# Optimization experiments

Measured on AMD Instinct MI355X. Metric: run time of the kernel, lower is better.

Reference implementation:

```python
import jax, jax.numpy as jnp
import numpy as np
from math import sqrt

B, S, D, H = 2, 2048, 1024, 16
HD = D // H


def setup_inputs() -> dict:
    key = jax.random.key(0)
    ks = jax.random.split(key, 5)
    std = 0.02
    return {
        "tensor_in": jax.random.normal(ks[0], (B, S, D), dtype=jnp.float32),
        "attention_mask": jnp.zeros((1, 1, S, S), dtype=jnp.float32),
        "Wq": jax.random.normal(ks[1], (D, D), dtype=jnp.float32) * std,
        "Wk": jax.random.normal(ks[2], (D, D), dtype=jnp.float32) * std,
        "Wv": jax.random.normal(ks[3], (D, D), dtype=jnp.float32) * std,
        "Wo": jax.random.normal(ks[4], (D, D), dtype=jnp.float32) * std,
    }


def reference(tensor_in, attention_mask, Wq, Wk, Wv, Wo):
    # nn.Linear(dim, dim, bias=False): y = x @ W.T, W is [out, in]
    q = tensor_in @ Wq.T  # [B,S,D]
    k = tensor_in @ Wk.T
    v = tensor_in @ Wv.T
    # split heads -> [B,H,S,HD]
    q = q.reshape(B, S, H, HD).transpose(0, 2, 1, 3)
    k = k.reshape(B, S, H, HD).transpose(0, 2, 1, 3)
    v = v.reshape(B, S, H, HD).transpose(0, 2, 1, 3)
    # scores [B,H,S,S]; note: mask added BEFORE scaling, scale = sqrt(full dim)
    scores = jnp.einsum("bhqd,bhkd->bhqk", q, k) + attention_mask
    weights = jax.nn.softmax(scores / sqrt(D), axis=-1)  # dropout = identity (eval)
    context = jnp.einsum("bhqk,bhkd->bhqd", weights, v)
    context = context.transpose(0, 2, 1, 3).reshape(B, S, D)
    return context @ Wo.T
```

## Files before the change

### kernel.cpp

```cpp
#include <hip/hip_runtime.h>

#define B_  2
#define S_  2048
#define D_  1024
#define H_  16
#define HD_ 64
#define M_  (B_*S_)

typedef __attribute__((ext_vector_type(8))) short  short8;
typedef __attribute__((ext_vector_type(4))) float  float4v;
typedef __attribute__((ext_vector_type(4))) int    int4v;
typedef __attribute__((ext_vector_type(4))) unsigned short ushort4v;

#define QSCALE 0.03125f

__device__ __forceinline__ unsigned short f_to_bf16bits(float f) {
    unsigned int x = __builtin_bit_cast(unsigned int, f);
    unsigned int lsb = (x >> 16) & 1u;
    x += 0x7fffu + lsb;
    return (unsigned short)(x >> 16);
}

__device__ __forceinline__ void async16(unsigned short* lds, const unsigned short* g) {
    __builtin_amdgcn_global_load_lds(
        (const __attribute__((address_space(1))) void*)g,
        (__attribute__((address_space(3))) void*)lds, 16, 0, 0);
}

__global__ __launch_bounds__(256) void cvt_bf16(
    const float* __restrict__ X,  const float* __restrict__ Wq,
    const float* __restrict__ Wk, const float* __restrict__ Wv,
    const float* __restrict__ Wo,
    unsigned short* __restrict__ Xb,  unsigned short* __restrict__ Wqb,
    unsigned short* __restrict__ Wkb, unsigned short* __restrict__ Wvb,
    unsigned short* __restrict__ Wob)
{
    const long t = (long)blockIdx.x * 256 + threadIdx.x;
    const long e = t * 8;
    const float* src; unsigned short* dst; long off;
    if      (e < 4194304) { src = X;  dst = Xb;  off = e; }
    else if (e < 5242880) { src = Wq; dst = Wqb; off = e - 4194304; }
    else if (e < 6291456) { src = Wk; dst = Wkb; off = e - 5242880; }
    else if (e < 7340032) { src = Wv; dst = Wvb; off = e - 6291456; }
    else                  { src = Wo; dst = Wob; off = e - 7340032; }
    float4v a = *(const float4v*)&src[off];
    float4v b = *(const float4v*)&src[off + 4];
    int4v o;
    o[0] = (int)f_to_bf16bits(a[0]) | ((int)f_to_bf16bits(a[1]) << 16);
    o[1] = (int)f_to_bf16bits(a[2]) | ((int)f_to_bf16bits(a[3]) << 16);
    o[2] = (int)f_to_bf16bits(b[0]) | ((int)f_to_bf16bits(b[1]) << 16);
    o[3] = (int)f_to_bf16bits(b[2]) | ((int)f_to_bf16bits(b[3]) << 16);
    *(int4v*)&dst[off] = o;
}

__global__ __launch_bounds__(256) void gemm_bt(
    const unsigned short* __restrict__ A,
    const unsigned short* __restrict__ B0,
    const unsigned short* __restrict__ B1,
    const unsigned short* __restrict__ B2,
    void* __restrict__ O0, void* __restrict__ O1, void* __restrict__ O2,
    int mode_base)
{
    const int K = 1024;
    const int z = blockIdx.z;
    const unsigned short* Bw = (z == 0) ? B0 : (z == 1) ? B1 : B2;
    void* Op                 = (z == 0) ? O0 : (z == 1) ? O1 : O2;
    const int mode = mode_base + z;

    __shared__ alignas(16) unsigned short As[128 * 32];
    __shared__ alignas(16) unsigned short Bs[128 * 32];

    const int tid  = threadIdx.x;
    const int wv   = tid >> 6;
    const int lane = tid & 63;
    const int wm   = wv >> 1, wn = wv & 1;
    const int q4   = lane >> 4, l15 = lane & 15;

    const int m0 = blockIdx.x * 128;
    const int n0 = blockIdx.y * 128;

    const int r0 = (wv * 2 + 0) * 16 + (lane >> 2);
    const int r1 = (wv * 2 + 1) * 16 + (lane >> 2);
    const int c0 = (((lane & 3) ^ (r0 & 3)) * 8);
    const int c1 = (((lane & 3) ^ (r1 & 3)) * 8);
    const unsigned short* gA0 = A  + (long)(m0 + r0) * K + c0;
    const unsigned short* gA1 = A  + (long)(m0 + r1) * K + c1;
    const unsigned short* gB0 = Bw + (long)(n0 + r0) * K + c0;
    const unsigned short* gB1 = Bw + (long)(n0 + r1) * K + c1;
    const int slot0 = (wv * 2 + 0) * 512;
    const int slot1 = (wv * 2 + 1) * 512;

    const int swz = (q4 ^ (l15 & 3)) * 8;
    int aoff[4], boff[4];
#pragma unroll
    for (int t = 0; t < 4; t++) {
        aoff[t] = (wm * 64 + t * 16 + l15) * 32 + swz;
        boff[t] = (wn * 64 + t * 16 + l15) * 32 + swz;
    }

    float4v acc[4][4];
#pragma unroll
    for (int i = 0; i < 4; i++)
#pragma unroll
        for (int j = 0; j < 4; j++) acc[i][j] = (float4v)0.0f;

    for (int k0 = 0; k0 < K; k0 += 32) {
        __syncthreads();
        async16(&As[slot0], gA0); async16(&As[slot1], gA1);
        async16(&Bs[slot0], gB0); async16(&Bs[slot1], gB1);
        gA0 += 32; gA1 += 32; gB0 += 32; gB1 += 32;
        __syncthreads();

        short8 afr[4], bfr[4];
#pragma unroll
        for (int mt = 0; mt < 4; mt++) afr[mt] = *(const short8*)&As[aoff[mt]];
#pragma unroll
        for (int nt = 0; nt < 4; nt++) bfr[nt] = *(const short8*)&Bs[boff[nt]];
#pragma unroll
        for (int mt = 0; mt < 4; mt++)
#pragma unroll
            for (int nt = 0; nt < 4; nt++)
                acc[mt][nt] = __builtin_amdgcn_mfma_f32_16x16x32_bf16(
                    afr[mt], bfr[nt], acc[mt][nt], 0, 0, 0);
    }

#pragma unroll
    for (int mt = 0; mt < 4; mt++)
#pragma unroll
        for (int nt = 0; nt < 4; nt++)
#pragma unroll
            for (int r = 0; r < 4; r++) {
                const int m = m0 + wm * 64 + mt * 16 + q4 * 4 + r;
                const int n = n0 + wn * 64 + nt * 16 + l15;
                float v = acc[mt][nt][r];
                if (mode == 3) {
                    ((float*)Op)[(long)m * D_ + n] = v;
                } else {
                    long off;
                    if (mode != 2)
                        off = ((long)((m >> 11) * H_ + (n >> 6)) * S_ + (m & 2047)) * HD_ + (n & 63);
                    else
                        off = ((long)((m >> 11) * H_ + (n >> 6)) * HD_ + (n & 63)) * S_ + (m & 2047);
                    if (mode == 0) v *= QSCALE;
                    ((unsigned short*)Op)[off] = f_to_bf16bits(v);
                }
            }
}

__global__ __launch_bounds__(256) void attn(
    const unsigned short* __restrict__ Q,
    const unsigned short* __restrict__ Kk,
    const unsigned short* __restrict__ Vt,
    const float* __restrict__ mask,
    unsigned short* __restrict__ ctx)
{
    __shared__ alignas(16) unsigned short Ks [64 * 72];
    __shared__ alignas(16) unsigned short Vts[64 * 72];
    __shared__ alignas(16) unsigned short Ps [4][16 * 72];

    const int tid  = threadIdx.x;
    const int wv   = tid >> 6;
    const int lane = tid & 63;
    const int q4   = lane >> 4, l15 = lane & 15;
    const int bh   = blockIdx.y;
    const int q0   = blockIdx.x * 64;

    const long head = (long)bh * S_ * HD_;

    const int qrow = q0 + wv * 16 + l15;
    short8 qfr[2];
    qfr[0] = *(const short8*)&Q[head + (long)qrow * HD_ + q4 * 8];
    qfr[1] = *(const short8*)&Q[head + (long)qrow * HD_ + 32 + q4 * 8];

    float l_acc[4];
#pragma unroll
    for (int r = 0; r < 4; r++) l_acc[r] = 0.0f;
    float4v oacc[4];
#pragma unroll
    for (int dt = 0; dt < 4; dt++) oacc[dt] = (float4v)0.0f;

    const int lrow = tid >> 3;
    const int lcol = (tid & 7) * 8;

    const float* mrow[4];
#pragma unroll
    for (int r = 0; r < 4; r++)
        mrow[r] = mask + (long)(q0 + wv * 16 + q4 * 4 + r) * S_ + l15;

    for (int k0 = 0; k0 < S_; k0 += 64) {
        __syncthreads();
        *(int4v*)&Ks [lrow * 72 + lcol]        = *(const int4v*)&Kk[head + (long)(k0 + lrow)      * HD_ + lcol];
        *(int4v*)&Ks [(lrow + 32) * 72 + lcol] = *(const int4v*)&Kk[head + (long)(k0 + lrow + 32) * HD_ + lcol];
        *(int4v*)&Vts[lrow * 72 + lcol]        = *(const int4v*)&Vt[head + (long)lrow        * S_ + k0 + lcol];
        *(int4v*)&Vts[(lrow + 32) * 72 + lcol] = *(const int4v*)&Vt[head + (long)(lrow + 32) * S_ + k0 + lcol];

        float mv[4][4];
#pragma unroll
        for (int nt = 0; nt < 4; nt++)
#pragma unroll
            for (int r = 0; r < 4; r++)
                mv[nt][r] = mrow[r][k0 + nt * 16];
        __syncthreads();

        float4v sfr[4];
#pragma unroll
        for (int nt = 0; nt < 4; nt++) {
            short8 kb0 = *(const short8*)&Ks[(nt * 16 + l15) * 72 + q4 * 8];
            short8 kb1 = *(const short8*)&Ks[(nt * 16 + l15) * 72 + 32 + q4 * 8];
            float4v s = (float4v)0.0f;
            s = __builtin_amdgcn_mfma_f32_16x16x32_bf16(qfr[0], kb0, s, 0, 0, 0);
            s = __builtin_amdgcn_mfma_f32_16x16x32_bf16(qfr[1], kb1, s, 0, 0, 0);
            sfr[nt] = s;
        }

#pragma unroll
        for (int nt = 0; nt < 4; nt++)
#pragma unroll
            for (int r = 0; r < 4; r++) {
                const float p = __expf(fmaf(mv[nt][r], QSCALE, sfr[nt][r]));
                l_acc[r] += p;
                Ps[wv][(q4 * 4 + r) * 72 + nt * 16 + l15] = f_to_bf16bits(p);
            }

        short8 pf0 = *(const short8*)&Ps[wv][l15 * 72 + q4 * 8];
        short8 pf1 = *(const short8*)&Ps[wv][l15 * 72 + 32 + q4 * 8];

#pragma unroll
        for (int dt = 0; dt < 4; dt++) {
            short8 vb0 = *(const short8*)&Vts[(dt * 16 + l15) * 72 + q4 * 8];
            short8 vb1 = *(const short8*)&Vts[(dt * 16 + l15) * 72 + 32 + q4 * 8];
            float4v o = oacc[dt];
            o = __builtin_amdgcn_mfma_f32_16x16x32_bf16(pf0, vb0, o, 0, 0, 0);
            o = __builtin_amdgcn_mfma_f32_16x16x32_bf16(pf1, vb1, o, 0, 0, 0);
            oacc[dt] = o;
        }
    }

#pragma unroll
    for (int r = 0; r < 4; r++) {
#pragma unroll
        for (int off = 1; off < 16; off <<= 1)
            l_acc[r] += __shfl_xor(l_acc[r], off);
    }

    const int b = bh >> 4, h = bh & 15;
#pragma unroll
    for (int dt = 0; dt < 4; dt++)
#pragma unroll
        for (int r = 0; r < 4; r++) {
            const int qg = q0 + wv * 16 + q4 * 4 + r;
            const int d  = dt * 16 + l15;
            const float v = oacc[dt][r] / l_acc[r];
            ctx[((long)(b * S_ + qg)) * D_ + h * HD_ + d] = f_to_bf16bits(v);
        }
}

extern "C" void kernel_launch(void* const* d_in, const int* in_sizes, int n_in,
                              void* d_out, int out_size, void* d_ws, size_t ws_size,
                              hipStream_t stream) {
    const float* X    = (const float*)d_in[0];
    const float* mask = (const float*)d_in[1];
    const float* Wq   = (const float*)d_in[2];
    const float* Wk   = (const float*)d_in[3];
    const float* Wv   = (const float*)d_in[4];
    const float* Wo   = (const float*)d_in[5];
    float* out        = (float*)d_out;

    unsigned short* ws = (unsigned short*)d_ws;
    unsigned short* qws  = ws;
    unsigned short* kws  = ws + 4194304;
    unsigned short* vtws = ws + 8388608;
    unsigned short* ctx  = ws + 12582912;
    unsigned short* Xb   = ws + 16777216;
    unsigned short* Wqb  = ws + 20971520;
    unsigned short* Wkb  = ws + 22020096;
    unsigned short* Wvb  = ws + 23068672;
    unsigned short* Wob  = ws + 24117248;

    cvt_bf16<<<dim3(4096), 256, 0, stream>>>(X, Wq, Wk, Wv, Wo, Xb, Wqb, Wkb, Wvb, Wob);
    gemm_bt<<<dim3(32, 8, 3), 256, 0, stream>>>(Xb, Wqb, Wkb, Wvb, qws, kws, vtws, 0);
    attn<<<dim3(32, 32, 1), 256, 0, stream>>>(qws, kws, vtws, mask, ctx);
    gemm_bt<<<dim3(32, 8, 1), 256, 0, stream>>>(ctx, Wob, Wob, Wob, out, out, out, 3);
}
```

Measured before the change: 253.9 us.

## Double-buffer attention K/V tiles with async LDS loads and swizzled layout

The attention kernel now prefetches the next K/V tile straight into a second LDS buffer with async global-to-LDS loads while computing on the current one. It replaces padded rows with XOR-swizzled 64-wide rows, applies the same swizzle to the P scratch, and prefetches the next mask values. This aims to hide global load latency and drop one barrier per iteration. Separately, the V projection GEMM swaps its operands so the transposed V output is written contiguously along the sequence dimension, at the cost of more index logic and LDS pressure.

```diff
diff --git a/kernel.cpp b/kernel.cpp
--- a/kernel.cpp
+++ b/kernel.cpp
@@ -63,9 +63,21 @@
 {
     const int K = 1024;
     const int z = blockIdx.z;
-    const unsigned short* Bw = (z == 0) ? B0 : (z == 1) ? B1 : B2;
-    void* Op                 = (z == 0) ? O0 : (z == 1) ? O1 : O2;
     const int mode = mode_base + z;
+    const unsigned short* Aop;
+    const unsigned short* Bop;
+    void* Op = (z == 0) ? O0 : (z == 1) ? O1 : O2;
+    int m0, n0;
+    if (mode == 2) {
+        Aop = B2; Bop = A;
+        m0 = blockIdx.y * 128;
+        n0 = blockIdx.x * 128;
+    } else {
+        Aop = A;
+        Bop = (z == 0) ? B0 : (z == 1) ? B1 : B2;
+        m0 = blockIdx.x * 128;
+        n0 = blockIdx.y * 128;
+    }
 
     __shared__ alignas(16) unsigned short As[128 * 32];
     __shared__ alignas(16) unsigned short Bs[128 * 32];
@@ -76,17 +88,14 @@
     const int wm   = wv >> 1, wn = wv & 1;
     const int q4   = lane >> 4, l15 = lane & 15;
 
-    const int m0 = blockIdx.x * 128;
-    const int n0 = blockIdx.y * 128;
-
     const int r0 = (wv * 2 + 0) * 16 + (lane >> 2);
     const int r1 = (wv * 2 + 1) * 16 + (lane >> 2);
     const int c0 = (((lane & 3) ^ (r0 & 3)) * 8);
     const int c1 = (((lane & 3) ^ (r1 & 3)) * 8);
-    const unsigned short* gA0 = A  + (long)(m0 + r0) * K + c0;
-    const unsigned short* gA1 = A  + (long)(m0 + r1) * K + c1;
-    const unsigned short* gB0 = Bw + (long)(n0 + r0) * K + c0;
-    const unsigned short* gB1 = Bw + (long)(n0 + r1) * K + c1;
+    const unsigned short* gA0 = Aop + (long)(m0 + r0) * K + c0;
+    const unsigned short* gA1 = Aop + (long)(m0 + r1) * K + c1;
+    const unsigned short* gB0 = Bop + (long)(n0 + r0) * K + c0;
+    const unsigned short* gB1 = Bop + (long)(n0 + r1) * K + c1;
     const int slot0 = (wv * 2 + 0) * 512;
     const int slot1 = (wv * 2 + 1) * 512;
 
@@ -135,12 +144,11 @@
                 float v = acc[mt][nt][r];
                 if (mode == 3) {
                     ((float*)Op)[(long)m * D_ + n] = v;
+                } else if (mode == 2) {
+                    const long off = (((long)(n >> 11) * H_ + (m >> 6)) * HD_ + (m & 63)) * S_ + (n & 2047);
+                    ((unsigned short*)Op)[off] = f_to_bf16bits(v);
                 } else {
-                    long off;
-                    if (mode != 2)
-                        off = ((long)((m >> 11) * H_ + (n >> 6)) * S_ + (m & 2047)) * HD_ + (n & 63);
-                    else
-                        off = ((long)((m >> 11) * H_ + (n >> 6)) * HD_ + (n & 63)) * S_ + (m & 2047);
+                    const long off = ((long)((m >> 11) * H_ + (n >> 6)) * S_ + (m & 2047)) * HD_ + (n & 63);
                     if (mode == 0) v *= QSCALE;
                     ((unsigned short*)Op)[off] = f_to_bf16bits(v);
                 }
@@ -154,9 +162,8 @@
     const float* __restrict__ mask,
     unsigned short* __restrict__ ctx)
 {
-    __shared__ alignas(16) unsigned short Ks [64 * 72];
-    __shared__ alignas(16) unsigned short Vts[64 * 72];
-    __shared__ alignas(16) unsigned short Ps [4][16 * 72];
+    __shared__ alignas(16) unsigned short KV[2][2][64 * 64];
+    __shared__ alignas(16) unsigned short Ps[4][16 * 64];
 
     const int tid  = threadIdx.x;
     const int wv   = tid >> 6;
@@ -179,61 +186,101 @@
 #pragma unroll
     for (int dt = 0; dt < 4; dt++) oacc[dt] = (float4v)0.0f;
 
-    const int lrow = tid >> 3;
-    const int lcol = (tid & 7) * 8;
+    const int srow = lane >> 3;
+    const int sch  = lane & 7;
+    const int row0 = wv * 16 + srow;
+    const int row1 = wv * 16 + 8 + srow;
+    const int cc0  = ((sch ^ (row0 & 7)) * 8);
+    const int cc1  = ((sch ^ (row1 & 7)) * 8);
+    const unsigned short* gK0 = Kk + head + (long)row0 * HD_ + cc0;
+    const unsigned short* gK1 = Kk + head + (long)row1 * HD_ + cc1;
+    const unsigned short* gV0 = Vt + head + (long)row0 * S_  + cc0;
+    const unsigned short* gV1 = Vt + head + (long)row1 * S_  + cc1;
+    const int ldsK0 = (wv * 16 + 0) * 64;
+    const int ldsK1 = (wv * 16 + 8) * 64;
 
     const float* mrow[4];
 #pragma unroll
     for (int r = 0; r < 4; r++)
         mrow[r] = mask + (long)(q0 + wv * 16 + q4 * 4 + r) * S_ + l15;
 
+    async16(&KV[0][0][ldsK0], gK0);
+    async16(&KV[0][0][ldsK1], gK1);
+    async16(&KV[0][1][ldsK0], gV0);
+    async16(&KV[0][1][ldsK1], gV1);
+    float mv[4][4];
+#pragma unroll
+    for (int nt = 0; nt < 4; nt++)
+#pragma unroll
+        for (int r = 0; r < 4; r++) mv[nt][r] = mrow[r][nt * 16];
+
+    const int pswz = (q4 & 1) * 4;
+    const int psl3 = l15 >> 3;
+
     for (int k0 = 0; k0 < S_; k0 += 64) {
+        const int buf = (k0 >> 6) & 1;
         __syncthreads();
-        *(int4v*)&Ks [lrow * 72 + lcol]        = *(const int4v*)&Kk[head + (long)(k0 + lrow)      * HD_ + lcol];
-        *(int4v*)&Ks [(lrow + 32) * 72 + lcol] = *(const int4v*)&Kk[head + (long)(k0 + lrow + 32) * HD_ + lcol];
-        *(int4v*)&Vts[lrow * 72 + lcol]        = *(const int4v*)&Vt[head + (long)lrow        * S_ + k0 + lcol];
-        *(int4v*)&Vts[(lrow + 32) * 72 + lcol] = *(const int4v*)&Vt[head + (long)(lrow + 32) * S_ + k0 + lcol];
-
-        float mv[4][4];
-#pragma unroll
-        for (int nt = 0; nt < 4; nt++)
-#pragma unroll
-            for (int r = 0; r < 4; r++)
-                mv[nt][r] = mrow[r][k0 + nt * 16];
-        __syncthreads();
+
+        if (k0 + 64 < S_) {
+            async16(&KV[buf ^ 1][0][ldsK0], gK0 + (long)(k0 + 64) * HD_);
+            async16(&KV[buf ^ 1][0][ldsK1], gK1 + (long)(k0 + 64) * HD_);
+            async16(&KV[buf ^ 1][1][ldsK0], gV0 + (k0 + 64));
+            async16(&KV[buf ^ 1][1][ldsK1], gV1 + (k0 + 64));
+        }
 
         float4v sfr[4];
 #pragma unroll
         for (int nt = 0; nt < 4; nt++) {
-            short8 kb0 = *(const short8*)&Ks[(nt * 16 + l15) * 72 + q4 * 8];
-            short8 kb1 = *(const short8*)&Ks[(nt * 16 + l15) * 72 + 32 + q4 * 8];
+            const int row = nt * 16 + l15;
+            const int p0 = ((q4     ^ (row & 7)) * 8);
+            const int p1 = (((4+q4) ^ (row & 7)) * 8);
+            short8 kb0 = *(const short8*)&KV[buf][0][row * 64 + p0];
+            short8 kb1 = *(const short8*)&KV[buf][0][row * 64 + p1];
             float4v s = (float4v)0.0f;
             s = __builtin_amdgcn_mfma_f32_16x16x32_bf16(qfr[0], kb0, s, 0, 0, 0);
             s = __builtin_amdgcn_mfma_f32_16x16x32_bf16(qfr[1], kb1, s, 0, 0, 0);
             sfr[nt] = s;
         }
 
+        float mvn[4][4];
+        const int knext = (k0 + 64 < S_) ? k0 + 64 : k0;
+#pragma unroll
+        for (int nt = 0; nt < 4; nt++)
+#pragma unroll
+            for (int r = 0; r < 4; r++) mvn[nt][r] = mrow[r][knext + nt * 16];
+
 #pragma unroll
         for (int nt = 0; nt < 4; nt++)
 #pragma unroll
             for (int r = 0; r < 4; r++) {
                 const float p = __expf(fmaf(mv[nt][r], QSCALE, sfr[nt][r]));
                 l_acc[r] += p;
-                Ps[wv][(q4 * 4 + r) * 72 + nt * 16 + l15] = f_to_bf16bits(p);
+                const int c8 = (nt * 2 + psl3) ^ (pswz + r);
+                Ps[wv][(q4 * 4 + r) * 64 + c8 * 8 + (l15 & 7)] = f_to_bf16bits(p);
             }
 
-        short8 pf0 = *(const short8*)&Ps[wv][l15 * 72 + q4 * 8];
-        short8 pf1 = *(const short8*)&Ps[wv][l15 * 72 + 32 + q4 * 8];
+        const int pp0 = ((q4     ^ (l15 & 7)) * 8);
+        const int pp1 = (((4+q4) ^ (l15 & 7)) * 8);
+        short8 pf0 = *(const short8*)&Ps[wv][l15 * 64 + pp0];
+        short8 pf1 = *(const short8*)&Ps[wv][l15 * 64 + pp1];
 
 #pragma unroll
         for (int dt = 0; dt < 4; dt++) {
-            short8 vb0 = *(const short8*)&Vts[(dt * 16 + l15) * 72 + q4 * 8];
-            short8 vb1 = *(const short8*)&Vts[(dt * 16 + l15) * 72 + 32 + q4 * 8];
+            const int row = dt * 16 + l15;
+            const int p0 = ((q4     ^ (row & 7)) * 8);
+            const int p1 = (((4+q4) ^ (row & 7)) * 8);
+            short8 vb0 = *(const short8*)&KV[buf][1][row * 64 + p0];
+            short8 vb1 = *(const short8*)&KV[buf][1][row * 64 + p1];
             float4v o = oacc[dt];
             o = __builtin_amdgcn_mfma_f32_16x16x32_bf16(pf0, vb0, o, 0, 0, 0);
             o = __builtin_amdgcn_mfma_f32_16x16x32_bf16(pf1, vb1, o, 0, 0, 0);
             oacc[dt] = o;
         }
+
+#pragma unroll
+        for (int nt = 0; nt < 4; nt++)
+#pragma unroll
+            for (int r = 0; r < 4; r++) mv[nt][r] = mvn[nt][r];
     }
 
 #pragma unroll
```

New measurement: 259.9 us. 2.4% more time.
